# Kernel tuning notes

Hardware: AMD Instinct MI355X
Metric: run time of the kernel (lower is better)

The kernel has to match this reference:

```python
import jax, jax.numpy as jnp
import numpy as np

H = 4          # global_attention_heads
NL = 32        # num_landmark_tokens
STRIDE = 16    # landmark_stride
D = 3072       # hidden_size
HD = D // H    # head_dim = 768
SCALE = 1.0 / np.sqrt(HD).astype(np.float32)


def _landmark_indices(seq_len: int) -> jnp.ndarray:
    # torch: arange(0, seq_len, stride); if >NL, index with linspace(0, n-1, NL).long() (truncation)
    idx = np.arange(0, seq_len, STRIDE, dtype=np.int64)
    if len(idx) > NL:
        sel = np.linspace(0, len(idx) - 1, NL).astype(np.int64)  # truncates like torch long cast
        idx = idx[sel]
    return jnp.asarray(idx)


def _attn(q_in, kv_in, Wq, bq, Wk, bk, Wv, bv, Wo, bo):
    # shared QKV/O projections, standard multi-head attention q_in -> kv_in
    B, Lq, _ = q_in.shape
    Lk = kv_in.shape[1]
    Q = (q_in @ Wq + bq).reshape(B, Lq, H, HD)
    K = (kv_in @ Wk + bk).reshape(B, Lk, H, HD)
    V = (kv_in @ Wv + bv).reshape(B, Lk, H, HD)
    scores = jnp.einsum('bqhd,bkhd->bhqk', Q, K) * SCALE
    w = jax.nn.softmax(scores, axis=-1)  # dropout is identity in eval
    ctx = jnp.einsum('bhqk,bkhd->bqhd', w, V).reshape(B, Lq, D)
    return ctx @ Wo + bo


def setup_inputs() -> dict:
    key = jax.random.key(0)
    ks = jax.random.split(key, 10)
    B, S = 2, 8192
    s = 1.0 / np.sqrt(D).astype(np.float32)
    return {
        'hidden_states': jax.random.normal(ks[0], (B, S, D), jnp.float32),
        'landmark_emb': jax.random.normal(ks[1], (NL, D), jnp.float32),
        'Wq': jax.random.normal(ks[2], (D, D), jnp.float32) * s,
        'bq': jnp.zeros((D,), jnp.float32),
        'Wk': jax.random.normal(ks[3], (D, D), jnp.float32) * s,
        'bk': jnp.zeros((D,), jnp.float32),
        'Wv': jax.random.normal(ks[4], (D, D), jnp.float32) * s,
        'bv': jnp.zeros((D,), jnp.float32),
        'Wo': jax.random.normal(ks[5], (D, D), jnp.float32) * s,
        'bo': jnp.zeros((D,), jnp.float32),
    }


def reference(hidden_states, landmark_emb, Wq, bq, Wk, bk, Wv, bv, Wo, bo):
    B, S, _ = hidden_states.shape
    li = _landmark_indices(S)  # [NL], static
    # gather landmarks + learned landmark embeddings
    landmark_tokens = hidden_states[:, li, :] + landmark_emb[None]  # [B, NL, D]
    # all tokens attend to 32 landmarks
    global_out = _attn(hidden_states, landmark_tokens, Wq, bq, Wk, bk, Wv, bv, Wo, bo)  # [B,S,D]
    # landmarks attend to all tokens
    landmark_out = _attn(landmark_tokens, hidden_states, Wq, bq, Wk, bk, Wv, bv, Wo, bo)  # [B,NL,D]
    # scatter landmark outputs back (index_copy-style, replaces python loop)
    updated = hidden_states.at[:, li, :].set(landmark_out)
    return updated + global_out
```

## Files before the change

kernel.cpp:

```cpp
#include <hip/hip_runtime.h>
#include <stdint.h>

#define S_LEN   8192
#define DMODEL  3072
#define HDIM    768
#define NLM     32
#define MTOK    16384
#define MV      16448
#define MP      16512
#define NQKV    9216
#define KDIM    3072
#define NKT     48
#define MTILES  65
#define SCALE_F 0.036084391824351615f

#define OFF_A    ((size_t)0)
#define OFF_WT   ((size_t)101449728)
#define OFF_QKV  ((size_t)176947200)
#define OFF_CTX  ((size_t)480116736)
#define OFF_BCAT ((size_t)581566464)
#define OFF_PART ((size_t)581615616)
#define OFF_KT   (OFF_PART)
#define OFF_VT   (OFF_PART + 393216)
#define OFF_ML2  (OFF_PART + 786432)
#define OFF_CP   (OFF_A)

#if defined(__has_builtin)
#if __has_builtin(__builtin_amdgcn_global_load_lds)
#define USE_GLL 1
#endif
#endif
#ifndef USE_GLL
#define USE_GLL 0
#endif

typedef __attribute__((ext_vector_type(8))) short bf8_t;
typedef __attribute__((ext_vector_type(4))) float f4_t;
typedef __attribute__((ext_vector_type(4))) short s4_t;
typedef __attribute__((ext_vector_type(4))) unsigned short us4_t;

__device__ __forceinline__ float b2f(unsigned short u) {
  unsigned x = ((unsigned)u) << 16;
  float f;
  __builtin_memcpy(&f, &x, 4);
  return f;
}
__device__ __forceinline__ unsigned short f2b(float f) {
  unsigned x;
  __builtin_memcpy(&x, &f, 4);
  x += 0x7fffu + ((x >> 16) & 1u);
  return (unsigned short)(x >> 16);
}
__device__ __forceinline__ void load12(const unsigned short* p, float* f) {
  s4_t v0 = *(const s4_t*)p;
  s4_t v1 = *(const s4_t*)(p + 4);
  s4_t v2 = *(const s4_t*)(p + 8);
#pragma unroll
  for (int e = 0; e < 4; ++e) {
    f[e]     = b2f((unsigned short)v0[e]);
    f[4 + e] = b2f((unsigned short)v1[e]);
    f[8 + e] = b2f((unsigned short)v2[e]);
  }
}
__device__ __forceinline__ void store12(unsigned short* p, const float* f) {
  us4_t a = {f2b(f[0]), f2b(f[1]), f2b(f[2]), f2b(f[3])};
  us4_t b = {f2b(f[4]), f2b(f[5]), f2b(f[6]), f2b(f[7])};
  us4_t c = {f2b(f[8]), f2b(f[9]), f2b(f[10]), f2b(f[11])};
  *(us4_t*)p = a;
  *(us4_t*)(p + 4) = b;
  *(us4_t*)(p + 8) = c;
}

__global__ __launch_bounds__(256) void build_bcat(const float* __restrict__ bq,
                                                  const float* __restrict__ bk,
                                                  const float* __restrict__ bv,
                                                  const float* __restrict__ bo,
                                                  float* __restrict__ bcat) {
  int n = blockIdx.x * 256 + threadIdx.x;
  float v = (n < 3072) ? bq[n] : (n < 6144) ? bk[n - 3072]
          : (n < 9216) ? bv[n - 6144] : bo[n - 9216];
  bcat[n] = v;
}

__global__ __launch_bounds__(256) void build_a(const float* __restrict__ hs,
                                               const float* __restrict__ lemb,
                                               unsigned short* __restrict__ A) {
  size_t idx = (size_t)blockIdx.x * 256 + threadIdx.x;
  size_t e = idx * 4;
  int row = (int)(e / DMODEL);
  int col = (int)(e - (size_t)row * DMODEL);
  f4_t v;
  if (row < MTOK) {
    v = *(const f4_t*)(hs + e);
  } else if (row < MV) {
    int r2 = row - MTOK;
    int b = r2 >> 5, j = r2 & 31;
    int sel = (j * 511) / 31;
    int li = sel * 16;
    f4_t a = *(const f4_t*)(hs + ((size_t)(b * S_LEN + li)) * DMODEL + col);
    f4_t c = *(const f4_t*)(lemb + (size_t)j * DMODEL + col);
    v = a + c;
  } else {
    v = (f4_t){0.f, 0.f, 0.f, 0.f};
  }
  us4_t o = {f2b(v[0]), f2b(v[1]), f2b(v[2]), f2b(v[3])};
  *(us4_t*)(A + e) = o;
}

__global__ __launch_bounds__(256) void wtrans4(const float* __restrict__ W0,
                                               const float* __restrict__ W1,
                                               const float* __restrict__ W2,
                                               const float* __restrict__ W3,
                                               unsigned short* __restrict__ Wt) {
  __shared__ float t[32][33];
  const float* Wsel[4] = {W0, W1, W2, W3};
  const float* W = Wsel[blockIdx.z];
  unsigned short* dst = Wt + (size_t)blockIdx.z * 3072 * KDIM;
  int n0 = blockIdx.x * 32, k0 = blockIdx.y * 32;
  int x = threadIdx.x, y = threadIdx.y;
#pragma unroll
  for (int i = 0; i < 4; ++i)
    t[y + i * 8][x] = W[(size_t)(k0 + y + i * 8) * DMODEL + n0 + x];
  __syncthreads();
#pragma unroll
  for (int i = 0; i < 4; ++i)
    dst[(size_t)(n0 + y + i * 8) * DMODEL + k0 + x] = f2b(t[x][y + i * 8]);
}

#if USE_GLL
#define GLL16(SRC, OFF)                                                        \
  __builtin_amdgcn_global_load_lds(                                           \
      (const __attribute__((address_space(1))) void*)(SRC),                   \
      (__attribute__((address_space(3))) void*)(lds + (OFF)), 16, 0, 0)
#else
#define GLL16(SRC, OFF)                                                        \
  (*(bf8_t*)(lds + (OFF) + (unsigned)(threadIdx.x & 63) * 16) = *(const bf8_t*)(SRC))
#endif

#define STG_A(TT, KH, DD)                                                      \
  do {                                                                         \
    const unsigned short* _s = gA0 + (size_t)(TT) * 64 + (KH) * 32;            \
    GLL16(_s, (unsigned)((DD) * 32768 + (KH) * 16384) + wl16);                 \
    GLL16(_s + (size_t)128 * KDIM,                                             \
          (unsigned)((DD) * 32768 + (KH) * 16384 + 8192) + wl16);              \
  } while (0)
#define STG_B(TT, KH, DD)                                                      \
  do {                                                                         \
    const unsigned short* _s = gB0 + (size_t)(TT) * 64 + (KH) * 32;            \
    GLL16(_s, (unsigned)(65536 + (DD) * 32768 + (KH) * 16384) + wl16);         \
    GLL16(_s + (size_t)128 * KDIM,                                             \
          (unsigned)(65536 + (DD) * 32768 + (KH) * 16384 + 8192) + wl16);      \
  } while (0)

#define LDA8(DD, KH, QM, MI)                                                   \
  (*(const bf8_t*)(lds + (DD) * 32768 + (KH) * 16384 + aBase + (QM) * 4096 +   \
                   (MI) * 1024))
#define LDB8(DD, KH, NI)                                                       \
  (*(const bf8_t*)(lds + (DD) * 32768 + (KH) * 16384 + bBase + (NI) * 1024))

#define MFMA16(Q, A0, A1, A2, A3, B0, B1, B2, B3)                              \
  do {                                                                         \
    __builtin_amdgcn_s_setprio(1);                                             \
    acc[(Q)+0][0] = __builtin_amdgcn_mfma_f32_16x16x32_bf16(A0, B0, acc[(Q)+0][0], 0, 0, 0); \
    acc[(Q)+1][0] = __builtin_amdgcn_mfma_f32_16x16x32_bf16(A1, B0, acc[(Q)+1][0], 0, 0, 0); \
    acc[(Q)+2][0] = __builtin_amdgcn_mfma_f32_16x16x32_bf16(A2, B0, acc[(Q)+2][0], 0, 0, 0); \
    acc[(Q)+3][0] = __builtin_amdgcn_mfma_f32_16x16x32_bf16(A3, B0, acc[(Q)+3][0], 0, 0, 0); \
    acc[(Q)+0][1] = __builtin_amdgcn_mfma_f32_16x16x32_bf16(A0, B1, acc[(Q)+0][1], 0, 0, 0); \
    acc[(Q)+1][1] = __builtin_amdgcn_mfma_f32_16x16x32_bf16(A1, B1, acc[(Q)+1][1], 0, 0, 0); \
    acc[(Q)+2][1] = __builtin_amdgcn_mfma_f32_16x16x32_bf16(A2, B1, acc[(Q)+2][1], 0, 0, 0); \
    acc[(Q)+3][1] = __builtin_amdgcn_mfma_f32_16x16x32_bf16(A3, B1, acc[(Q)+3][1], 0, 0, 0); \
    acc[(Q)+0][2] = __builtin_amdgcn_mfma_f32_16x16x32_bf16(A0, B2, acc[(Q)+0][2], 0, 0, 0); \
    acc[(Q)+1][2] = __builtin_amdgcn_mfma_f32_16x16x32_bf16(A1, B2, acc[(Q)+1][2], 0, 0, 0); \
    acc[(Q)+2][2] = __builtin_amdgcn_mfma_f32_16x16x32_bf16(A2, B2, acc[(Q)+2][2], 0, 0, 0); \
    acc[(Q)+3][2] = __builtin_amdgcn_mfma_f32_16x16x32_bf16(A3, B2, acc[(Q)+3][2], 0, 0, 0); \
    acc[(Q)+0][3] = __builtin_amdgcn_mfma_f32_16x16x32_bf16(A0, B3, acc[(Q)+0][3], 0, 0, 0); \
    acc[(Q)+1][3] = __builtin_amdgcn_mfma_f32_16x16x32_bf16(A1, B3, acc[(Q)+1][3], 0, 0, 0); \
    acc[(Q)+2][3] = __builtin_amdgcn_mfma_f32_16x16x32_bf16(A2, B3, acc[(Q)+2][3], 0, 0, 0); \
    acc[(Q)+3][3] = __builtin_amdgcn_mfma_f32_16x16x32_bf16(A3, B3, acc[(Q)+3][3], 0, 0, 0); \
    __builtin_amdgcn_s_setprio(0);                                             \
  } while (0)

__global__ __launch_bounds__(512, 2) void gemm256(const unsigned short* __restrict__ A,
                                                  const unsigned short* __restrict__ Bt,
                                                  const float* __restrict__ bias,
                                                  unsigned short* __restrict__ C,
                                                  int Mvalid, int N, int Ntiles) {
  extern __shared__ char lds[];
  const int tid = threadIdx.x;
  const int lane = tid & 63;
  const int wave = tid >> 6;
  const int WM = wave >> 2;
  const int WN = wave & 3;
  const int row16 = lane & 15, quad = lane >> 4;

  int nwg = (int)gridDim.x;
  int orig = (int)blockIdx.x;
  int q = nwg >> 3, r = nwg & 7;
  int xcd = orig & 7, lin = orig >> 3;
  int wg = (xcd < r ? xcd * (q + 1) : r * (q + 1) + (xcd - r) * q) + lin;

  int g = wg / (MTILES * 8);
  int w2 = wg - g * (MTILES * 8);
  int Ng = Ntiles - g * 8;
  int m_, nl;
  if (Ng >= 8) { m_ = w2 >> 3; nl = w2 & 7; }
  else         { m_ = w2 / Ng; nl = w2 - m_ * Ng; }
  const int tileM = m_ * 256;
  const int tileN = (g * 8 + nl) * 256;

  const int srow2 = tid >> 2;
  const int scq = (tid & 3) ^ ((srow2 >> 1) & 3);
  const unsigned short* gA0 = A + (size_t)(tileM + srow2) * KDIM + scq * 8;
  const unsigned short* gB0 = Bt + (size_t)(tileN + srow2) * KDIM + scq * 8;
  const unsigned wl16 = (unsigned)(tid & 448) * 16;

  const unsigned co = (unsigned)((quad * 16) ^ (((row16 >> 1) & 3) << 4));
  const unsigned aBase = (unsigned)(WM * 8192 + row16 * 64) + co;
  const unsigned bBase = 65536u + (unsigned)(WN * 4096 + row16 * 64) + co;

  f4_t acc[8][4];
#pragma unroll
  for (int a = 0; a < 8; ++a)
#pragma unroll
    for (int b = 0; b < 4; ++b) acc[a][b] = (f4_t){0.f, 0.f, 0.f, 0.f};

  STG_B(0, 0, 0); STG_A(0, 0, 0); STG_B(0, 1, 0); STG_A(0, 1, 0);
  STG_B(1, 0, 1); STG_A(1, 0, 1); STG_B(1, 1, 1);
  asm volatile("s_waitcnt vmcnt(6)" ::: "memory");
  __builtin_amdgcn_s_barrier();

#pragma unroll 2
  for (int t = 0; t < NKT; ++t) {
    const int d = t & 1;
    {
      bf8_t a0 = LDA8(d, 0, 0, 0), a1 = LDA8(d, 0, 0, 1),
            a2 = LDA8(d, 0, 0, 2), a3 = LDA8(d, 0, 0, 3);
      bf8_t b0 = LDB8(d, 0, 0), b1 = LDB8(d, 0, 1),
            b2 = LDB8(d, 0, 2), b3 = LDB8(d, 0, 3);
      if (t + 1 < NKT) STG_A(t + 1, 1, d ^ 1);
      __builtin_amdgcn_s_barrier();
      asm volatile("s_waitcnt lgkmcnt(0)");
      MFMA16(0, a0, a1, a2, a3, b0, b1, b2, b3);
      __builtin_amdgcn_s_barrier();
      bf8_t a4 = LDA8(d, 0, 1, 0), a5 = LDA8(d, 0, 1, 1),
            a6 = LDA8(d, 0, 1, 2), a7 = LDA8(d, 0, 1, 3);
      if (t + 2 < NKT) STG_B(t + 2, 0, d);
      __builtin_amdgcn_s_barrier();
      asm volatile("s_waitcnt lgkmcnt(0)");
      MFMA16(4, a4, a5, a6, a7, b0, b1, b2, b3);
      __builtin_amdgcn_s_barrier();
    }
    {
      bf8_t a0 = LDA8(d, 1, 0, 0), a1 = LDA8(d, 1, 0, 1),
            a2 = LDA8(d, 1, 0, 2), a3 = LDA8(d, 1, 0, 3);
      bf8_t b0 = LDB8(d, 1, 0), b1 = LDB8(d, 1, 1),
            b2 = LDB8(d, 1, 2), b3 = LDB8(d, 1, 3);
      if (t + 2 < NKT) STG_A(t + 2, 0, d);
      __builtin_amdgcn_s_barrier();
      asm volatile("s_waitcnt lgkmcnt(0)");
      MFMA16(0, a0, a1, a2, a3, b0, b1, b2, b3);
      __builtin_amdgcn_s_barrier();
      bf8_t a4 = LDA8(d, 1, 1, 0), a5 = LDA8(d, 1, 1, 1),
            a6 = LDA8(d, 1, 1, 2), a7 = LDA8(d, 1, 1, 3);
      if (t + 2 < NKT) STG_B(t + 2, 1, d);
      __builtin_amdgcn_s_barrier();
      asm volatile("s_waitcnt lgkmcnt(0)");
      MFMA16(4, a4, a5, a6, a7, b0, b1, b2, b3);
      if (t + 2 < NKT) asm volatile("s_waitcnt vmcnt(6)" ::: "memory");
      else             asm volatile("s_waitcnt vmcnt(0)" ::: "memory");
      __builtin_amdgcn_s_barrier();
    }
  }

  float bv_[4];
#pragma unroll
  for (int ni = 0; ni < 4; ++ni) bv_[ni] = bias[tileN + WN * 64 + ni * 16 + row16];
#pragma unroll
  for (int mi = 0; mi < 8; ++mi) {
#pragma unroll
    for (int i = 0; i < 4; ++i) {
      int grow = tileM + WM * 128 + mi * 16 + quad * 4 + i;
      if (grow < Mvalid) {
        size_t base = (size_t)grow * N + tileN + WN * 64 + row16;
#pragma unroll
        for (int ni = 0; ni < 4; ++ni)
          C[base + ni * 16] = f2b(acc[mi][ni][i] + bv_[ni]);
      }
    }
  }
}

__global__ __launch_bounds__(256) void kv_prep(const unsigned short* __restrict__ QKV,
                                               unsigned short* __restrict__ KT,
                                               unsigned short* __restrict__ VT) {
  int idx = blockIdx.x * 256 + threadIdx.x;
  if (idx < 24576) {
    int bh = idx / 3072, i = idx % 3072;
    int b = bh >> 2, h = bh & 3;
    int j = i & 31, c = i >> 5;
    bf8_t v = *(const bf8_t*)(QKV + (size_t)(MTOK + b * NLM + j) * NQKV + DMODEL +
                              h * HDIM + c * 8);
    *(bf8_t*)(KT + (size_t)bh * 24576 + (size_t)(c * 32 + j) * 8) = v;
  } else {
    int i2 = idx - 24576;
    int bh = i2 / 3072, r = i2 % 3072;
    int b = bh >> 2, h = bh & 3;
    int d = r >> 2, slot = r & 3;
    unsigned short vals[8];
#pragma unroll
    for (int e = 0; e < 8; ++e)
      vals[e] = QKV[(size_t)(MTOK + b * NLM + slot * 8 + e) * NQKV + 2 * DMODEL +
                    h * HDIM + d];
    unsigned short* p = VT + (size_t)bh * 24576 + (size_t)d * 32 + slot * 8;
    *(us4_t*)p = (us4_t){vals[0], vals[1], vals[2], vals[3]};
    *(us4_t*)(p + 4) = (us4_t){vals[4], vals[5], vals[6], vals[7]};
  }
}

__global__ __launch_bounds__(256, 2) void glob_attn(const unsigned short* __restrict__ QKV,
                                                    const unsigned short* __restrict__ KT,
                                                    const unsigned short* __restrict__ VT,
                                                    unsigned short* __restrict__ CTX) {
  __shared__ unsigned short P_s[4][32][32];
  const int tid = threadIdx.x;
  const int lane = tid & 63;
  const int w = tid >> 6;
  const int row16 = lane & 15, quad = lane >> 4;

  const int qt = blockIdx.x & 63;
  const int h = (blockIdx.x >> 6) & 3;
  const int b = blockIdx.x >> 8;
  const int bh = b * 4 + h;
  const int rowbase = b * S_LEN + qt * 128 + w * 32;

  const unsigned short* KTb = KT + (size_t)bh * 24576;
  const unsigned short* VTb = VT + (size_t)bh * 24576;

  f4_t sc[2][2];
#pragma unroll
  for (int mi = 0; mi < 2; ++mi)
#pragma unroll
    for (int ni = 0; ni < 2; ++ni) sc[mi][ni] = (f4_t){0.f, 0.f, 0.f, 0.f};

#pragma unroll
  for (int kt = 0; kt < 24; ++kt) {
    bf8_t kb0 = *(const bf8_t*)(KTb + (size_t)((kt * 4 + quad) * 32 + row16) * 8);
    bf8_t kb1 = *(const bf8_t*)(KTb + (size_t)((kt * 4 + quad) * 32 + 16 + row16) * 8);
    bf8_t qa0 = *(const bf8_t*)(QKV + (size_t)(rowbase + row16) * NQKV + h * HDIM +
                                kt * 32 + quad * 8);
    bf8_t qa1 = *(const bf8_t*)(QKV + (size_t)(rowbase + 16 + row16) * NQKV + h * HDIM +
                                kt * 32 + quad * 8);
    sc[0][0] = __builtin_amdgcn_mfma_f32_16x16x32_bf16(qa0, kb0, sc[0][0], 0, 0, 0);
    sc[0][1] = __builtin_amdgcn_mfma_f32_16x16x32_bf16(qa0, kb1, sc[0][1], 0, 0, 0);
    sc[1][0] = __builtin_amdgcn_mfma_f32_16x16x32_bf16(qa1, kb0, sc[1][0], 0, 0, 0);
    sc[1][1] = __builtin_amdgcn_mfma_f32_16x16x32_bf16(qa1, kb1, sc[1][1], 0, 0, 0);
  }

#pragma unroll
  for (int mi = 0; mi < 2; ++mi) {
#pragma unroll
    for (int i = 0; i < 4; ++i) {
      float s0 = sc[mi][0][i] * SCALE_F;
      float s1 = sc[mi][1][i] * SCALE_F;
      float mx = fmaxf(s0, s1);
#pragma unroll
      for (int off = 8; off; off >>= 1) mx = fmaxf(mx, __shfl_xor(mx, off));
      float p0 = __expf(s0 - mx), p1 = __expf(s1 - mx);
      float sum = p0 + p1;
#pragma unroll
      for (int off = 8; off; off >>= 1) sum += __shfl_xor(sum, off);
      float inv = 1.f / sum;
      int rr = mi * 16 + quad * 4 + i;
      P_s[w][rr][row16] = f2b(p0 * inv);
      P_s[w][rr][16 + row16] = f2b(p1 * inv);
    }
  }
  __syncthreads();

  bf8_t pa0 = *(const bf8_t*)&P_s[w][row16][quad * 8];
  bf8_t pa1 = *(const bf8_t*)&P_s[w][16 + row16][quad * 8];
  unsigned short* ctxb = CTX + (size_t)rowbase * DMODEL + h * HDIM;

#pragma unroll
  for (int dch = 0; dch < 12; ++dch) {
    bf8_t vb[4];
#pragma unroll
    for (int ni = 0; ni < 4; ++ni)
      vb[ni] = *(const bf8_t*)(VTb + (size_t)(dch * 64 + ni * 16 + row16) * 32 + quad * 8);
#pragma unroll
    for (int mi = 0; mi < 2; ++mi) {
      bf8_t pa = mi ? pa1 : pa0;
#pragma unroll
      for (int ni = 0; ni < 4; ++ni) {
        f4_t c = __builtin_amdgcn_mfma_f32_16x16x32_bf16(
            pa, vb[ni], (f4_t){0.f, 0.f, 0.f, 0.f}, 0, 0, 0);
#pragma unroll
        for (int i = 0; i < 4; ++i)
          ctxb[(size_t)(mi * 16 + quad * 4 + i) * DMODEL + dch * 64 + ni * 16 + row16] =
              f2b(c[i]);
      }
    }
  }
}

__global__ __launch_bounds__(256, 2) void lm_attn_part(const unsigned short* __restrict__ QKV,
                                                       float* __restrict__ ctxpart,
                                                       float* __restrict__ mlpart) {
  int wid = blockIdx.x * 4 + (threadIdx.x >> 6);
  int lane = threadIdx.x & 63;
  int jg = wid & 3, kc = (wid >> 2) & 63, h = (wid >> 8) & 3, b = wid >> 10;

  float qreg[8][12];
#pragma unroll
  for (int jj = 0; jj < 8; ++jj)
    load12(QKV + (size_t)(MTOK + b * NLM + jg * 8 + jj) * NQKV + h * HDIM + lane * 12,
           qreg[jj]);

  float m[8], l[8], ctx[8][12];
#pragma unroll
  for (int jj = 0; jj < 8; ++jj) {
    m[jj] = -1e30f;
    l[jj] = 0.f;
#pragma unroll
    for (int e = 0; e < 12; ++e) ctx[jj][e] = 0.f;
  }

  for (int k = kc * 128; k < kc * 128 + 128; ++k) {
    size_t row = (size_t)(b * S_LEN + k);
    float kv[12], vv[12];
    load12(QKV + row * NQKV + DMODEL + h * HDIM + lane * 12, kv);
    float s[8];
#pragma unroll
    for (int jj = 0; jj < 8; ++jj) {
      float p = 0.f;
#pragma unroll
      for (int e = 0; e < 12; ++e) p += qreg[jj][e] * kv[e];
      s[jj] = p;
    }
#pragma unroll
    for (int jj = 0; jj < 8; ++jj) {
#pragma unroll
      for (int off = 32; off; off >>= 1) s[jj] += __shfl_xor(s[jj], off);
      s[jj] *= SCALE_F;
    }
    load12(QKV + row * NQKV + 2 * DMODEL + h * HDIM + lane * 12, vv);
#pragma unroll
    for (int jj = 0; jj < 8; ++jj) {
      if (s[jj] <= m[jj]) {
        float pp = __expf(s[jj] - m[jj]);
        l[jj] += pp;
#pragma unroll
        for (int e = 0; e < 12; ++e) ctx[jj][e] += pp * vv[e];
      } else {
        float al = __expf(m[jj] - s[jj]);
        m[jj] = s[jj];
        l[jj] = l[jj] * al + 1.f;
#pragma unroll
        for (int e = 0; e < 12; ++e) ctx[jj][e] = ctx[jj][e] * al + vv[e];
      }
    }
  }

#pragma unroll
  for (int jj = 0; jj < 8; ++jj) {
    int p = (((b * 4 + h) * 32) + (jg * 8 + jj)) * 64 + kc;
    float* cp = ctxpart + (size_t)p * HDIM + lane * 12;
#pragma unroll
    for (int e = 0; e < 12; ++e) cp[e] = ctx[jj][e];
    if (lane == 0) {
      mlpart[p * 2] = m[jj];
      mlpart[p * 2 + 1] = l[jj];
    }
  }
}

__global__ __launch_bounds__(256) void lm_combine(const float* __restrict__ ctxpart,
                                                  const float* __restrict__ mlpart,
                                                  unsigned short* __restrict__ CTX) {
  int wid = blockIdx.x * 4 + (threadIdx.x >> 6);
  int lane = threadIdx.x & 63;
  int j = wid & 31, h = (wid >> 5) & 3, b = wid >> 7;
  int base = wid * 64;
  float mk = mlpart[(base + lane) * 2];
  float lk = mlpart[(base + lane) * 2 + 1];
  float mm = mk;
#pragma unroll
  for (int off = 32; off; off >>= 1) mm = fmaxf(mm, __shfl_xor(mm, off));
  float al = __expf(mk - mm);
  float ls = al * lk;
#pragma unroll
  for (int off = 32; off; off >>= 1) ls += __shfl_xor(ls, off);

  float ctx[12];
#pragma unroll
  for (int e = 0; e < 12; ++e) ctx[e] = 0.f;
  for (int kc = 0; kc < 64; ++kc) {
    float a = __shfl(al, kc);
    const float* cp = ctxpart + (size_t)(base + kc) * HDIM + lane * 12;
#pragma unroll
    for (int e = 0; e < 12; ++e) ctx[e] += a * cp[e];
  }
  float inv = 1.f / ls;
#pragma unroll
  for (int e = 0; e < 12; ++e) ctx[e] *= inv;
  store12(CTX + (size_t)(MTOK + b * NLM + j) * DMODEL + h * HDIM + lane * 12, ctx);
}

__global__ __launch_bounds__(256) void compose(const float* __restrict__ hs,
                                               const unsigned short* __restrict__ PROJ,
                                               float* __restrict__ out) {
  size_t idx = (size_t)blockIdx.x * 256 + threadIdx.x;
  size_t e = idx * 4;
  int row = (int)(e / DMODEL);
  int col = (int)(e - (size_t)row * DMODEL);
  int b = row >> 13, s = row & (S_LEN - 1);

  us4_t g4 = *(const us4_t*)(PROJ + (size_t)row * DMODEL + col);
  int j = -1;
  if ((s & 15) == 0) {
    int sel = s >> 4;
    int jc = (sel * 31 + 510) / 511;
    if (jc < 32 && (jc * 511) / 31 == sel) j = jc;
  }
  f4_t base;
  if (j >= 0) {
    us4_t l4 = *(const us4_t*)(PROJ + (size_t)(MTOK + b * NLM + j) * DMODEL + col);
    base = (f4_t){b2f(l4[0]), b2f(l4[1]), b2f(l4[2]), b2f(l4[3])};
  } else {
    base = *(const f4_t*)(hs + e);
  }
  f4_t o = {base[0] + b2f(g4[0]), base[1] + b2f(g4[1]),
            base[2] + b2f(g4[2]), base[3] + b2f(g4[3])};
  *(f4_t*)(out + e) = o;
}

extern "C" void kernel_launch(void* const* d_in, const int* in_sizes, int n_in,
                              void* d_out, int out_size, void* d_ws, size_t ws_size,
                              hipStream_t stream) {
  const float* hs   = (const float*)d_in[0];
  const float* lemb = (const float*)d_in[1];
  const float* Wq   = (const float*)d_in[2];
  const float* bq   = (const float*)d_in[3];
  const float* Wk   = (const float*)d_in[4];
  const float* bk   = (const float*)d_in[5];
  const float* Wv   = (const float*)d_in[6];
  const float* bv   = (const float*)d_in[7];
  const float* Wo   = (const float*)d_in[8];
  const float* bo   = (const float*)d_in[9];
  float* out = (float*)d_out;
  char* ws = (char*)d_ws;

  unsigned short* A    = (unsigned short*)(ws + OFF_A);
  unsigned short* Wt   = (unsigned short*)(ws + OFF_WT);
  unsigned short* QKV  = (unsigned short*)(ws + OFF_QKV);
  unsigned short* CTX  = (unsigned short*)(ws + OFF_CTX);
  float*          bcat = (float*)(ws + OFF_BCAT);
  unsigned short* KT   = (unsigned short*)(ws + OFF_KT);
  unsigned short* VT   = (unsigned short*)(ws + OFF_VT);
  float*          ml   = (float*)(ws + OFF_ML2);
  float*          cpart= (float*)(ws + OFF_CP);
  unsigned short* PROJ = (unsigned short*)(ws + OFF_A);

  static bool attr_set = false;
  if (!attr_set) {
    (void)hipFuncSetAttribute(reinterpret_cast<const void*>(gemm256),
                              hipFuncAttributeMaxDynamicSharedMemorySize, 131072);
    attr_set = true;
  }

  build_bcat<<<dim3(48), dim3(256), 0, stream>>>(bq, bk, bv, bo, bcat);
  build_a<<<dim3(49536), dim3(256), 0, stream>>>(hs, lemb, A);
  wtrans4<<<dim3(96, 96, 4), dim3(32, 8), 0, stream>>>(Wq, Wk, Wv, Wo, Wt);

  gemm256<<<dim3(65 * 36), dim3(512), 131072, stream>>>(A, Wt, bcat, QKV, MV, NQKV, 36);

  kv_prep<<<dim3(192), dim3(256), 0, stream>>>(QKV, KT, VT);
  glob_attn<<<dim3(512), dim3(256), 0, stream>>>(QKV, KT, VT, CTX);
  lm_attn_part<<<dim3(512), dim3(256), 0, stream>>>(QKV, cpart, ml);
  lm_combine<<<dim3(64), dim3(256), 0, stream>>>(cpart, ml, CTX);

  gemm256<<<dim3(65 * 12), dim3(512), 131072, stream>>>(
      CTX, Wt + (size_t)9216 * KDIM, bcat + 9216, PROJ, MV, DMODEL, 12);

  compose<<<dim3(49152), dim3(256), 0, stream>>>(hs, PROJ, out);
}
```

Measured before the change: 2.048 ms.

## Split landmark rows into small GEMM and fuse compose into output projection epilogue

The 64 landmark rows are moved out of the large tiled GEMMs into a separate small MFMA kernel, so the main GEMMs cover exactly 64 M-tiles instead of 65 mostly-empty ones. The output-projection GEMM epilogue now adds the residual (hidden states, or the projected landmark row at landmark positions) and writes fp32 output directly. This drops the separate compose pass and the bf16 PROJ round trip through memory. In exchange it adds two small low-occupancy launches, and the epilogue makes uncoalesced strided fp32 stores and reads.

```diff
diff --git a/kernel.cpp b/kernel.cpp
--- a/kernel.cpp
+++ b/kernel.cpp
@@ -11,7 +11,7 @@
 #define NQKV    9216
 #define KDIM    3072
 #define NKT     48
-#define MTILES  65
+#define MTILES  64
 #define SCALE_F 0.036084391824351615f
 
 #define OFF_A    ((size_t)0)
@@ -23,6 +23,7 @@
 #define OFF_KT   (OFF_PART)
 #define OFF_VT   (OFF_PART + 393216)
 #define OFF_ML2  (OFF_PART + 786432)
+#define OFF_PLM  (OFF_PART + 917504)
 #define OFF_CP   (OFF_A)
 
 #if defined(__has_builtin)
@@ -125,6 +126,47 @@
 #pragma unroll
   for (int i = 0; i < 4; ++i)
     dst[(size_t)(n0 + y + i * 8) * DMODEL + k0 + x] = f2b(t[x][y + i * 8]);
+}
+
+__global__ __launch_bounds__(256) void lm_gemm(const unsigned short* __restrict__ A64,
+                                               const unsigned short* __restrict__ Bt,
+                                               const float* __restrict__ bias,
+                                               unsigned short* __restrict__ C64,
+                                               int N, int ldc) {
+  int wv = blockIdx.x * 4 + (threadIdx.x >> 6);
+  int lane = threadIdx.x & 63;
+  int row16 = lane & 15, quad = lane >> 4;
+  int n0 = wv * 32;
+  if (n0 >= N) return;
+
+  f4_t acc[4][2];
+#pragma unroll
+  for (int mi = 0; mi < 4; ++mi) {
+    acc[mi][0] = (f4_t){0.f, 0.f, 0.f, 0.f};
+    acc[mi][1] = (f4_t){0.f, 0.f, 0.f, 0.f};
+  }
+  for (int kt = 0; kt < 96; ++kt) {
+    int k = kt * 32 + quad * 8;
+    bf8_t b0 = *(const bf8_t*)(Bt + (size_t)(n0 + row16) * KDIM + k);
+    bf8_t b1 = *(const bf8_t*)(Bt + (size_t)(n0 + 16 + row16) * KDIM + k);
+#pragma unroll
+    for (int mi = 0; mi < 4; ++mi) {
+      bf8_t a = *(const bf8_t*)(A64 + (size_t)(mi * 16 + row16) * KDIM + k);
+      acc[mi][0] = __builtin_amdgcn_mfma_f32_16x16x32_bf16(a, b0, acc[mi][0], 0, 0, 0);
+      acc[mi][1] = __builtin_amdgcn_mfma_f32_16x16x32_bf16(a, b1, acc[mi][1], 0, 0, 0);
+    }
+  }
+#pragma unroll
+  for (int mi = 0; mi < 4; ++mi)
+#pragma unroll
+    for (int i = 0; i < 4; ++i) {
+      int r = mi * 16 + quad * 4 + i;
+#pragma unroll
+      for (int nl = 0; nl < 2; ++nl) {
+        int col = n0 + nl * 16 + row16;
+        C64[(size_t)r * ldc + col] = f2b(acc[mi][nl][i] + bias[col]);
+      }
+    }
 }
 
 #if USE_GLL
@@ -184,7 +226,10 @@
                                                   const unsigned short* __restrict__ Bt,
                                                   const float* __restrict__ bias,
                                                   unsigned short* __restrict__ C,
-                                                  int Mvalid, int N, int Ntiles) {
+                                                  const float* __restrict__ hs,
+                                                  const unsigned short* __restrict__ plm,
+                                                  float* __restrict__ outF,
+                                                  int N, int Ntiles) {
   extern __shared__ char lds[];
   const int tid = threadIdx.x;
   const int lane = tid & 63;
@@ -275,12 +320,37 @@
   float bv_[4];
 #pragma unroll
   for (int ni = 0; ni < 4; ++ni) bv_[ni] = bias[tileN + WN * 64 + ni * 16 + row16];
-#pragma unroll
-  for (int mi = 0; mi < 8; ++mi) {
-#pragma unroll
-    for (int i = 0; i < 4; ++i) {
-      int grow = tileM + WM * 128 + mi * 16 + quad * 4 + i;
-      if (grow < Mvalid) {
+
+  if (outF) {
+#pragma unroll
+    for (int mi = 0; mi < 8; ++mi) {
+#pragma unroll
+      for (int i = 0; i < 4; ++i) {
+        int grow = tileM + WM * 128 + mi * 16 + quad * 4 + i;
+        int s = grow & (S_LEN - 1), b = grow >> 13;
+        int j = -1;
+        if ((s & 15) == 0) {
+          int sel = s >> 4;
+          int jc = (sel * 31 + 510) / 511;
+          if (jc < 32 && (jc * 511) / 31 == sel) j = jc;
+        }
+        const float* hrow = hs + (size_t)grow * DMODEL;
+        size_t obase = (size_t)grow * DMODEL;
+#pragma unroll
+        for (int ni = 0; ni < 4; ++ni) {
+          int col = tileN + WN * 64 + ni * 16 + row16;
+          float base = (j >= 0) ? b2f(plm[(size_t)(b * 32 + j) * DMODEL + col])
+                                : hrow[col];
+          outF[obase + col] = base + acc[mi][ni][i] + bv_[ni];
+        }
+      }
+    }
+  } else {
+#pragma unroll
+    for (int mi = 0; mi < 8; ++mi) {
+#pragma unroll
+      for (int i = 0; i < 4; ++i) {
+        int grow = tileM + WM * 128 + mi * 16 + quad * 4 + i;
         size_t base = (size_t)grow * N + tileN + WN * 64 + row16;
 #pragma unroll
         for (int ni = 0; ni < 4; ++ni)
@@ -506,34 +576,6 @@
   store12(CTX + (size_t)(MTOK + b * NLM + j) * DMODEL + h * HDIM + lane * 12, ctx);
 }
 
-__global__ __launch_bounds__(256) void compose(const float* __restrict__ hs,
-                                               const unsigned short* __restrict__ PROJ,
-                                               float* __restrict__ out) {
-  size_t idx = (size_t)blockIdx.x * 256 + threadIdx.x;
-  size_t e = idx * 4;
-  int row = (int)(e / DMODEL);
-  int col = (int)(e - (size_t)row * DMODEL);
-  int b = row >> 13, s = row & (S_LEN - 1);
-
-  us4_t g4 = *(const us4_t*)(PROJ + (size_t)row * DMODEL + col);
-  int j = -1;
-  if ((s & 15) == 0) {
-    int sel = s >> 4;
-    int jc = (sel * 31 + 510) / 511;
-    if (jc < 32 && (jc * 511) / 31 == sel) j = jc;
-  }
-  f4_t base;
-  if (j >= 0) {
-    us4_t l4 = *(const us4_t*)(PROJ + (size_t)(MTOK + b * NLM + j) * DMODEL + col);
-    base = (f4_t){b2f(l4[0]), b2f(l4[1]), b2f(l4[2]), b2f(l4[3])};
-  } else {
-    base = *(const f4_t*)(hs + e);
-  }
-  f4_t o = {base[0] + b2f(g4[0]), base[1] + b2f(g4[1]),
-            base[2] + b2f(g4[2]), base[3] + b2f(g4[3])};
-  *(f4_t*)(out + e) = o;
-}
-
 extern "C" void kernel_launch(void* const* d_in, const int* in_sizes, int n_in,
                               void* d_out, int out_size, void* d_ws, size_t ws_size,
                               hipStream_t stream) {
@@ -558,8 +600,8 @@
   unsigned short* KT   = (unsigned short*)(ws + OFF_KT);
   unsigned short* VT   = (unsigned short*)(ws + OFF_VT);
   float*          ml   = (float*)(ws + OFF_ML2);
+  unsigned short* plm  = (unsigned short*)(ws + OFF_PLM);
   float*          cpart= (float*)(ws + OFF_CP);
-  unsigned short* PROJ = (unsigned short*)(ws + OFF_A);
 
   static bool attr_set = false;
   if (!attr_set) {
@@ -572,15 +614,21 @@
   build_a<<<dim3(49536), dim3(256), 0, stream>>>(hs, lemb, A);
   wtrans4<<<dim3(96, 96, 4), dim3(32, 8), 0, stream>>>(Wq, Wk, Wv, Wo, Wt);
 
-  gemm256<<<dim3(65 * 36), dim3(512), 131072, stream>>>(A, Wt, bcat, QKV, MV, NQKV, 36);
+  gemm256<<<dim3(64 * 36), dim3(512), 131072, stream>>>(
+      A, Wt, bcat, QKV, nullptr, nullptr, nullptr, NQKV, 36);
+  lm_gemm<<<dim3(72), dim3(256), 0, stream>>>(
+      A + (size_t)MTOK * KDIM, Wt, bcat, QKV + (size_t)MTOK * NQKV, NQKV, NQKV);
 
   kv_prep<<<dim3(192), dim3(256), 0, stream>>>(QKV, KT, VT);
   glob_attn<<<dim3(512), dim3(256), 0, stream>>>(QKV, KT, VT, CTX);
   lm_attn_part<<<dim3(512), dim3(256), 0, stream>>>(QKV, cpart, ml);
   lm_combine<<<dim3(64), dim3(256), 0, stream>>>(cpart, ml, CTX);
 
-  gemm256<<<dim3(65 * 12), dim3(512), 131072, stream>>>(
-      CTX, Wt + (size_t)9216 * KDIM, bcat + 9216, PROJ, MV, DMODEL, 12);
-
-  compose<<<dim3(49152), dim3(256), 0, stream>>>(hs, PROJ, out);
-}
+  lm_gemm<<<dim3(24), dim3(256), 0, stream>>>(
+      CTX + (size_t)MTOK * DMODEL, Wt + (size_t)9216 * KDIM, bcat + 9216,
+      plm, DMODEL, DMODEL);
+
+  gemm256<<<dim3(64 * 12), dim3(512), 131072, stream>>>(
+      CTX, Wt + (size_t)9216 * KDIM, bcat + 9216, nullptr, hs, plm, out,
+      DMODEL, 12);
+}
```

Measured after the change: 2.089 ms. 2.0% more time.
